# Optimization experiments

Measured on AMD Instinct MI355X. Metric: run time of the kernel, lower is better.

The kernel has to match this reference:

```python
import jax, jax.numpy as jnp
import numpy as np
from jax import lax

B = 16384
BN_EPS = 1e-5


def setup_inputs() -> dict:
    key = jax.random.key(0)
    ks = jax.random.split(key, 6)
    x = jax.random.normal(ks[0], (B, 1, 28, 28), jnp.float32)
    conv_w = jax.random.normal(ks[1], (4, 1, 3, 3), jnp.float32) * 0.2
    bn_gamma = jnp.ones((4,), jnp.float32)
    bn_beta = jnp.zeros((4,), jnp.float32)
    bn_mean = jnp.zeros((4,), jnp.float32)
    bn_var = jnp.ones((4,), jnp.float32)
    var_params = jax.random.normal(ks[2], (4,), jnp.float32)
    lin_w = jax.random.normal(ks[3], (10, 784), jnp.float32) * 0.03
    lin_b = jnp.zeros((10,), jnp.float32)
    return {"x": x, "conv_w": conv_w, "bn_gamma": bn_gamma, "bn_beta": bn_beta,
            "bn_mean": bn_mean, "bn_var": bn_var, "var_params": var_params,
            "lin_w": lin_w, "lin_b": lin_b}


def _ry_w0(s, theta):
    # apply RY(theta) to wire 0 (axis -2) of real state s[..., 2, 2]
    c, si = jnp.cos(theta * 0.5), jnp.sin(theta * 0.5)
    R = jnp.stack([jnp.stack([c, -si]), jnp.stack([si, c])])
    return jnp.einsum('ij,...jk->...ik', R, s)


def _ry_w1(s, theta):
    # apply RY(theta) to wire 1 (axis -1)
    c, si = jnp.cos(theta * 0.5), jnp.sin(theta * 0.5)
    R = jnp.stack([jnp.stack([c, -si]), jnp.stack([si, c])])
    return jnp.einsum('ij,...kj->...ki', R, s)


def _quantum_features(img, v):
    # img: [B, 28, 28] -> features [B, 196*4] (patch-major, 4 expvals each)
    b = img.shape[0]
    p = img.reshape(b, 14, 2, 14, 2).transpose(0, 1, 3, 2, 4)  # [B,14,14,2,2]
    # encoding RYs on same wire compose: angles a = p0+p2 (wire0), b = p1+p3 (wire1)
    ha = (p[..., 0, 0] + p[..., 1, 0]) * 0.5
    hb = (p[..., 0, 1] + p[..., 1, 1]) * 0.5
    w0 = jnp.stack([jnp.cos(ha), jnp.sin(ha)], axis=-1)
    w1 = jnp.stack([jnp.cos(hb), jnp.sin(hb)], axis=-1)
    s = w0[..., :, None] * w1[..., None, :]  # real statevector [B,14,14,2,2]
    # CNOT(control=0, target=1): flip wire1 where wire0 == 1
    s = jnp.stack([s[..., 0, :], s[..., 1, ::-1]], axis=-2)
    s = _ry_w0(s, v[0])
    s = _ry_w1(s, v[1])
    # CNOT(control=1, target=0): flip wire0 where wire1 == 1
    s = jnp.stack([s[..., :, 0], s[..., ::-1, 1]], axis=-1)
    s = _ry_w0(s, v[2])
    s = _ry_w1(s, v[3])
    z0 = jnp.sum(s[..., 0, :] ** 2 - s[..., 1, :] ** 2, axis=-1)
    z1 = jnp.sum(s[..., :, 0] ** 2 - s[..., :, 1] ** 2, axis=-1)
    x0 = 2.0 * jnp.sum(s[..., 0, :] * s[..., 1, :], axis=-1)
    x1 = 2.0 * jnp.sum(s[..., :, 0] * s[..., :, 1], axis=-1)
    return jnp.stack([z0, z1, x0, x1], axis=-1).reshape(b, -1)  # [B,784]


def reference(x, conv_w, bn_gamma, bn_beta, bn_mean, bn_var, var_params, lin_w, lin_b):
    b = x.shape[0]
    # classical branch: conv(s=2,p=1) -> BN (eval) -> ReLU -> flatten
    h = lax.conv_general_dilated(x, conv_w, window_strides=(2, 2),
                                 padding=((1, 1), (1, 1)))  # [B,4,14,14]
    inv = bn_gamma / jnp.sqrt(bn_var + BN_EPS)
    h = h * inv[None, :, None, None] + (bn_beta - bn_mean * inv)[None, :, None, None]
    h = jnp.maximum(h, 0.0)
    cls_out = h.reshape(b, -1)  # [B,784]
    # quantum branch over 2x2 patches
    q_out = _quantum_features(x[:, 0], var_params)  # [B,784]
    fused = cls_out + q_out
    logits = fused @ lin_w.T + lin_b
    return jax.nn.log_softmax(logits, axis=-1)
```

## Files before the change

kernel.cpp:

```cpp
#include <hip/hip_runtime.h>
#include <math.h>


#define NW 4
#define IMG_STRIDE 36
#define IMG_WORDS (29 * 36)

__device__ __forceinline__ void lds_fence() {
    asm volatile("s_waitcnt lgkmcnt(0)" ::: "memory");
}

__device__ __forceinline__ float wave64_sum(float x) {
    int v;
    v = __builtin_amdgcn_update_dpp(0, __float_as_int(x), 0x111, 0xf, 0xf, true); x += __int_as_float(v);
    v = __builtin_amdgcn_update_dpp(0, __float_as_int(x), 0x112, 0xf, 0xf, true); x += __int_as_float(v);
    v = __builtin_amdgcn_update_dpp(0, __float_as_int(x), 0x114, 0xf, 0xf, true); x += __int_as_float(v);
    v = __builtin_amdgcn_update_dpp(0, __float_as_int(x), 0x118, 0xf, 0xf, true); x += __int_as_float(v);
    v = __builtin_amdgcn_update_dpp(0, __float_as_int(x), 0x142, 0xa, 0xf, true); x += __int_as_float(v);
    v = __builtin_amdgcn_update_dpp(0, __float_as_int(x), 0x143, 0xc, 0xf, true); x += __int_as_float(v);
    return __int_as_float(__builtin_amdgcn_readlane(__float_as_int(x), 63));
}

__global__ __launch_bounds__(256, 4)
void quanv_fused(const float* __restrict__ x,
                 const float* __restrict__ conv_w,
                 const float* __restrict__ bn_gamma,
                 const float* __restrict__ bn_beta,
                 const float* __restrict__ bn_mean,
                 const float* __restrict__ bn_var,
                 const float* __restrict__ var_params,
                 const float* __restrict__ lin_w,
                 const float* __restrict__ lin_b,
                 float* __restrict__ out, int B)
{
    __shared__ __align__(16) float simg[NW][IMG_WORDS];
    __shared__ __align__(16) float scls[NW][784];

    const int tid  = threadIdx.x;
    const int wave = tid >> 6;
    const int lane = tid & 63;
    const int sample = blockIdx.x * NW + wave;
    const bool active = (sample < B);

    float* im = simg[wave];

    if (lane < 36) im[lane] = 0.f;
    if (lane < 28) im[(lane + 1) * IMG_STRIDE + 3] = 0.f;

    if (active) {
        const float4* xs = (const float4*)(x + (size_t)sample * 784);
        #pragma unroll
        for (int t = 0; t < 4; ++t) {
            int g = lane + t * 64;
            if (g < 196) {
                float4 v = xs[g];
                int row  = (unsigned)g / 7u;
                int colb = (g - row * 7) * 4;
                *(float4*)&im[(row + 1) * IMG_STRIDE + 4 + colb] = v;
            }
        }
    }

    float w[36];
    #pragma unroll
    for (int k = 0; k < 36; ++k) w[k] = conv_w[k];
    float inv[4], addc[4];
    #pragma unroll
    for (int c = 0; c < 4; ++c) {
        float iv = bn_gamma[c] * rsqrtf(bn_var[c] + 1e-5f);
        inv[c]  = iv;
        addc[c] = bn_beta[c] - bn_mean[c] * iv;
    }
    float cv[4], sv[4];
    #pragma unroll
    for (int k = 0; k < 4; ++k) __sincosf(var_params[k] * 0.5f, &sv[k], &cv[k]);

    lds_fence();

    float4 qf[4];
    #pragma unroll
    for (int t = 0; t < 4; ++t) qf[t] = make_float4(0.f, 0.f, 0.f, 0.f);

    if (active) {
        #pragma unroll
        for (int t = 0; t < 4; ++t) {
            int p = lane + t * 64;
            if (p < 196) {
                int i = (unsigned)p / 14u;
                int j = p - i * 14;
                int base = (2 * i) * IMG_STRIDE + 3 + 2 * j;
                float a00 = im[base + 0],                a01 = im[base + 1],                a02 = im[base + 2];
                float a10 = im[base + IMG_STRIDE + 0],   a11 = im[base + IMG_STRIDE + 1],   a12 = im[base + IMG_STRIDE + 2];
                float a20 = im[base + 2*IMG_STRIDE + 0], a21 = im[base + 2*IMG_STRIDE + 1], a22 = im[base + 2*IMG_STRIDE + 2];

                #pragma unroll
                for (int c = 0; c < 4; ++c) {
                    float h = w[c*9+0]*a00 + w[c*9+1]*a01 + w[c*9+2]*a02
                            + w[c*9+3]*a10 + w[c*9+4]*a11 + w[c*9+5]*a12
                            + w[c*9+6]*a20 + w[c*9+7]*a21 + w[c*9+8]*a22;
                    h = h * inv[c] + addc[c];
                    scls[wave][c * 196 + p] = fmaxf(h, 0.f);
                }

                float ha = 0.5f * (a11 + a21);
                float hb = 0.5f * (a12 + a22);
                float c0, s0, c1, s1;
                __sincosf(ha, &s0, &c0);
                __sincosf(hb, &s1, &c1);
                float m00 = c0*c1, m01 = c0*s1;
                float m10 = s0*s1, m11 = s0*c1;
                float t00 = cv[0]*m00 - sv[0]*m10, t01 = cv[0]*m01 - sv[0]*m11;
                float t10 = sv[0]*m00 + cv[0]*m10, t11 = sv[0]*m01 + cv[0]*m11;
                float u00 = cv[1]*t00 - sv[1]*t01, u01 = sv[1]*t00 + cv[1]*t01;
                float u10 = cv[1]*t10 - sv[1]*t11, u11 = sv[1]*t10 + cv[1]*t11;
                float tmp = u01; u01 = u11; u11 = tmp;
                float p00 = cv[2]*u00 - sv[2]*u10, p01 = cv[2]*u01 - sv[2]*u11;
                float p10 = sv[2]*u00 + cv[2]*u10, p11 = sv[2]*u01 + cv[2]*u11;
                float q00 = cv[3]*p00 - sv[3]*p01, q01 = sv[3]*p00 + cv[3]*p01;
                float q10 = cv[3]*p10 - sv[3]*p11, q11 = sv[3]*p10 + cv[3]*p11;

                float z0 = q00*q00 + q01*q01 - q10*q10 - q11*q11;
                float z1 = q00*q00 + q10*q10 - q01*q01 - q11*q11;
                float x0 = 2.f * (q00*q10 + q01*q11);
                float x1 = 2.f * (q00*q01 + q10*q11);
                qf[t] = make_float4(z0, z1, x0, x1);
            }
        }
    }

    lds_fence();

    if (active) {
        const float4* lw4 = (const float4*)lin_w;
        float ps[10];
        #pragma unroll
        for (int o = 0; o < 10; ++o) ps[o] = 0.f;

        #pragma unroll
        for (int t = 0; t < 4; ++t) {
            int p  = lane + t * 64;
            int pc = (p < 196) ? p : 195;
            float m = (p < 196) ? 1.f : 0.f;
            float4 cl = *(const float4*)&scls[wave][4 * pc];
            float4 f = make_float4((cl.x + qf[t].x) * m, (cl.y + qf[t].y) * m,
                                   (cl.z + qf[t].z) * m, (cl.w + qf[t].w) * m);
            #pragma unroll
            for (int o = 0; o < 10; ++o) {
                float4 wv = lw4[o * 196 + pc];
                ps[o] += f.x * wv.x + f.y * wv.y + f.z * wv.z + f.w * wv.w;
            }
        }

        float lg[10];
        #pragma unroll
        for (int o = 0; o < 10; ++o) lg[o] = wave64_sum(ps[o]) + lin_b[o];

        float mx = lg[0];
        #pragma unroll
        for (int o = 1; o < 10; ++o) mx = fmaxf(mx, lg[o]);
        float se = 0.f;
        #pragma unroll
        for (int o = 0; o < 10; ++o) se += __expf(lg[o] - mx);
        float ls = __logf(se);

        if (lane < 10) {
            float v = lg[0];
            #pragma unroll
            for (int o = 1; o < 10; ++o) v = (lane == o) ? lg[o] : v;
            out[(size_t)sample * 10 + lane] = v - mx - ls;
        }
    }
}

extern "C" void kernel_launch(void* const* d_in, const int* in_sizes, int n_in,
                              void* d_out, int out_size, void* d_ws, size_t ws_size,
                              hipStream_t stream) {
    const float* x          = (const float*)d_in[0];
    const float* conv_w     = (const float*)d_in[1];
    const float* bn_gamma   = (const float*)d_in[2];
    const float* bn_beta    = (const float*)d_in[3];
    const float* bn_mean    = (const float*)d_in[4];
    const float* bn_var     = (const float*)d_in[5];
    const float* var_params = (const float*)d_in[6];
    const float* lin_w      = (const float*)d_in[7];
    const float* lin_b      = (const float*)d_in[8];
    float* out = (float*)d_out;

    const int B = in_sizes[0] / 784;
    const int blocks = (B + NW - 1) / NW;
    quanv_fused<<<blocks, 256, 0, stream>>>(x, conv_w, bn_gamma, bn_beta, bn_mean,
                                            bn_var, var_params, lin_w, lin_b, out, B);
}
```

Measured before the change: 119.6 us.

## Process two samples per wave with fp16 LDS weights and dot2 reductions

Each wave now handles two samples, one per 32-lane half, and halves the block count. The linear weights are converted to fp16 in LDS once per block and combined with fdot2, replacing per-lane global float loads. The image is read directly from global memory with padding masks instead of being staged in LDS. Conv and quantum features are stored in fp16, and the final reduction uses a 32-lane DPP sum. The fp16 features and weights add precision loss, and each block pays for its own copy of the lin_w conversion.

```diff
diff --git a/kernel.cpp b/kernel.cpp
--- a/kernel.cpp
+++ b/kernel.cpp
@@ -3,22 +3,30 @@
 
 
 #define NW 4
-#define IMG_STRIDE 36
-#define IMG_WORDS (29 * 36)
-
-__device__ __forceinline__ void lds_fence() {
-    asm volatile("s_waitcnt lgkmcnt(0)" ::: "memory");
-}
-
-__device__ __forceinline__ float wave64_sum(float x) {
+#define SCLS_STRIDE 794
+
+typedef __fp16 h2 __attribute__((ext_vector_type(2)));
+typedef __fp16 h4 __attribute__((ext_vector_type(4)));
+
+#if __has_builtin(__builtin_amdgcn_fdot2)
+#define FDOT2(a, b, c) __builtin_amdgcn_fdot2((a), (b), (c), false)
+#else
+__device__ __forceinline__ float FDOT2(h2 a, h2 b, float c) {
+    return (float)a.x * (float)b.x + (float)a.y * (float)b.y + c;
+}
+#endif
+
+__device__ __forceinline__ float2 red32x2(float x) {
     int v;
     v = __builtin_amdgcn_update_dpp(0, __float_as_int(x), 0x111, 0xf, 0xf, true); x += __int_as_float(v);
     v = __builtin_amdgcn_update_dpp(0, __float_as_int(x), 0x112, 0xf, 0xf, true); x += __int_as_float(v);
     v = __builtin_amdgcn_update_dpp(0, __float_as_int(x), 0x114, 0xf, 0xf, true); x += __int_as_float(v);
     v = __builtin_amdgcn_update_dpp(0, __float_as_int(x), 0x118, 0xf, 0xf, true); x += __int_as_float(v);
     v = __builtin_amdgcn_update_dpp(0, __float_as_int(x), 0x142, 0xa, 0xf, true); x += __int_as_float(v);
-    v = __builtin_amdgcn_update_dpp(0, __float_as_int(x), 0x143, 0xc, 0xf, true); x += __int_as_float(v);
-    return __int_as_float(__builtin_amdgcn_readlane(__float_as_int(x), 63));
+    float2 r;
+    r.x = __int_as_float(__builtin_amdgcn_readlane(__float_as_int(x), 31));
+    r.y = __int_as_float(__builtin_amdgcn_readlane(__float_as_int(x), 63));
+    return r;
 }
 
 __global__ __launch_bounds__(256, 4)
@@ -33,30 +41,31 @@
                  const float* __restrict__ lin_b,
                  float* __restrict__ out, int B)
 {
-    __shared__ __align__(16) float simg[NW][IMG_WORDS];
-    __shared__ __align__(16) float scls[NW][784];
+    __shared__ __align__(16) __fp16 lwh[7840];
+    __shared__ __align__(16) __fp16 sclsAll[NW * 2 * SCLS_STRIDE];
 
     const int tid  = threadIdx.x;
     const int wave = tid >> 6;
     const int lane = tid & 63;
-    const int sample = blockIdx.x * NW + wave;
-    const bool active = (sample < B);
-
-    float* im = simg[wave];
-
-    if (lane < 36) im[lane] = 0.f;
-    if (lane < 28) im[(lane + 1) * IMG_STRIDE + 3] = 0.f;
-
-    if (active) {
-        const float4* xs = (const float4*)(x + (size_t)sample * 784);
+    const int half = lane >> 5;
+    const int l32  = lane & 31;
+
+    const int s  = blockIdx.x * (NW * 2) + wave * 2 + half;
+    const int sc = (s < B) ? s : (B - 1);
+    const float* xs = x + (size_t)sc * 784;
+    __fp16* myscls = &sclsAll[(wave * 2 + half) * SCLS_STRIDE];
+
+    {
+        const float4* src = (const float4*)lin_w;
         #pragma unroll
-        for (int t = 0; t < 4; ++t) {
-            int g = lane + t * 64;
-            if (g < 196) {
-                float4 v = xs[g];
-                int row  = (unsigned)g / 7u;
-                int colb = (g - row * 7) * 4;
-                *(float4*)&im[(row + 1) * IMG_STRIDE + 4 + colb] = v;
+        for (int t = 0; t < 8; ++t) {
+            int i = tid + t * 256;
+            if (i < 1960) {
+                float4 v = src[i];
+                h2 a = __builtin_amdgcn_cvt_pkrtz(v.x, v.y);
+                h2 b = __builtin_amdgcn_cvt_pkrtz(v.z, v.w);
+                h4 w4 = { a.x, a.y, b.x, b.y };
+                *(h4*)&lwh[4 * i] = w4;
             }
         }
     }
@@ -75,100 +84,118 @@
     #pragma unroll
     for (int k = 0; k < 4; ++k) __sincosf(var_params[k] * 0.5f, &sv[k], &cv[k]);
 
-    lds_fence();
-
-    float4 qf[4];
-    #pragma unroll
-    for (int t = 0; t < 4; ++t) qf[t] = make_float4(0.f, 0.f, 0.f, 0.f);
-
-    if (active) {
-        #pragma unroll
-        for (int t = 0; t < 4; ++t) {
-            int p = lane + t * 64;
-            if (p < 196) {
-                int i = (unsigned)p / 14u;
-                int j = p - i * 14;
-                int base = (2 * i) * IMG_STRIDE + 3 + 2 * j;
-                float a00 = im[base + 0],                a01 = im[base + 1],                a02 = im[base + 2];
-                float a10 = im[base + IMG_STRIDE + 0],   a11 = im[base + IMG_STRIDE + 1],   a12 = im[base + IMG_STRIDE + 2];
-                float a20 = im[base + 2*IMG_STRIDE + 0], a21 = im[base + 2*IMG_STRIDE + 1], a22 = im[base + 2*IMG_STRIDE + 2];
-
-                #pragma unroll
-                for (int c = 0; c < 4; ++c) {
-                    float h = w[c*9+0]*a00 + w[c*9+1]*a01 + w[c*9+2]*a02
-                            + w[c*9+3]*a10 + w[c*9+4]*a11 + w[c*9+5]*a12
-                            + w[c*9+6]*a20 + w[c*9+7]*a21 + w[c*9+8]*a22;
-                    h = h * inv[c] + addc[c];
-                    scls[wave][c * 196 + p] = fmaxf(h, 0.f);
-                }
-
-                float ha = 0.5f * (a11 + a21);
-                float hb = 0.5f * (a12 + a22);
-                float c0, s0, c1, s1;
-                __sincosf(ha, &s0, &c0);
-                __sincosf(hb, &s1, &c1);
-                float m00 = c0*c1, m01 = c0*s1;
-                float m10 = s0*s1, m11 = s0*c1;
-                float t00 = cv[0]*m00 - sv[0]*m10, t01 = cv[0]*m01 - sv[0]*m11;
-                float t10 = sv[0]*m00 + cv[0]*m10, t11 = sv[0]*m01 + cv[0]*m11;
-                float u00 = cv[1]*t00 - sv[1]*t01, u01 = sv[1]*t00 + cv[1]*t01;
-                float u10 = cv[1]*t10 - sv[1]*t11, u11 = sv[1]*t10 + cv[1]*t11;
-                float tmp = u01; u01 = u11; u11 = tmp;
-                float p00 = cv[2]*u00 - sv[2]*u10, p01 = cv[2]*u01 - sv[2]*u11;
-                float p10 = sv[2]*u00 + cv[2]*u10, p11 = sv[2]*u01 + cv[2]*u11;
-                float q00 = cv[3]*p00 - sv[3]*p01, q01 = sv[3]*p00 + cv[3]*p01;
-                float q10 = cv[3]*p10 - sv[3]*p11, q11 = sv[3]*p10 + cv[3]*p11;
-
-                float z0 = q00*q00 + q01*q01 - q10*q10 - q11*q11;
-                float z1 = q00*q00 + q10*q10 - q01*q01 - q11*q11;
-                float x0 = 2.f * (q00*q10 + q01*q11);
-                float x1 = 2.f * (q00*q01 + q10*q11);
-                qf[t] = make_float4(z0, z1, x0, x1);
+    h2 qh[7][2];
+    #pragma unroll
+    for (int t = 0; t < 7; ++t) {
+        int p = l32 + 32 * t;
+        bool act = (p < 196);
+        int pc = act ? p : 195;
+        unsigned i = (unsigned)pc / 14u;
+        int j = pc - (int)i * 14;
+        int omid = (int)(2 * i) * 28 + 2 * j;
+
+        float2 Rm = *(const float2*)(xs + omid);
+        float2 Rb = *(const float2*)(xs + omid + 28);
+        int ot = omid - 28; ot = (ot > 0) ? ot : 0;
+        float2 Rt = *(const float2*)(xs + ot);
+        int olt = omid - 30; olt = (olt > 0) ? olt : 0;
+        float2 Lt = *(const float2*)(xs + olt);
+        int olm = omid - 2; olm = (olm > 0) ? olm : 0;
+        float2 Lm = *(const float2*)(xs + olm);
+        float2 Lb = *(const float2*)(xs + olm + 28);
+
+        float mt = (i > 0) ? 1.f : 0.f;
+        float ml = (j > 0) ? 1.f : 0.f;
+        float a00 = Lt.y * (mt * ml), a01 = Rt.x * mt, a02 = Rt.y * mt;
+        float a10 = Lm.y * ml,        a11 = Rm.x,      a12 = Rm.y;
+        float a20 = Lb.y * ml,        a21 = Rb.x,      a22 = Rb.y;
+
+        if (act) {
+            #pragma unroll
+            for (int c = 0; c < 4; ++c) {
+                float h = w[c*9+0]*a00 + w[c*9+1]*a01 + w[c*9+2]*a02
+                        + w[c*9+3]*a10 + w[c*9+4]*a11 + w[c*9+5]*a12
+                        + w[c*9+6]*a20 + w[c*9+7]*a21 + w[c*9+8]*a22;
+                h = h * inv[c] + addc[c];
+                myscls[c * 196 + pc] = (__fp16)fmaxf(h, 0.f);
             }
         }
-    }
-
-    lds_fence();
-
-    if (active) {
-        const float4* lw4 = (const float4*)lin_w;
-        float ps[10];
+
+        float ha = 0.5f * (a11 + a21);
+        float hb = 0.5f * (a12 + a22);
+        float c0, s0, c1, s1;
+        __sincosf(ha, &s0, &c0);
+        __sincosf(hb, &s1, &c1);
+        float m00 = c0*c1, m01 = c0*s1;
+        float m10 = s0*s1, m11 = s0*c1;
+        float t00 = cv[0]*m00 - sv[0]*m10, t01 = cv[0]*m01 - sv[0]*m11;
+        float t10 = sv[0]*m00 + cv[0]*m10, t11 = sv[0]*m01 + cv[0]*m11;
+        float u00 = cv[1]*t00 - sv[1]*t01, u01 = sv[1]*t00 + cv[1]*t01;
+        float u10 = cv[1]*t10 - sv[1]*t11, u11 = sv[1]*t10 + cv[1]*t11;
+        float tmp = u01; u01 = u11; u11 = tmp;
+        float p00 = cv[2]*u00 - sv[2]*u10, p01 = cv[2]*u01 - sv[2]*u11;
+        float p10 = sv[2]*u00 + cv[2]*u10, p11 = sv[2]*u01 + cv[2]*u11;
+        float q00 = cv[3]*p00 - sv[3]*p01, q01 = sv[3]*p00 + cv[3]*p01;
+        float q10 = cv[3]*p10 - sv[3]*p11, q11 = sv[3]*p10 + cv[3]*p11;
+
+        float z0 = q00*q00 + q01*q01 - q10*q10 - q11*q11;
+        float z1 = q00*q00 + q10*q10 - q01*q01 - q11*q11;
+        float x0 = 2.f * (q00*q10 + q01*q11);
+        float x1 = 2.f * (q00*q01 + q10*q11);
+        qh[t][0] = __builtin_amdgcn_cvt_pkrtz(z0, z1);
+        qh[t][1] = __builtin_amdgcn_cvt_pkrtz(x0, x1);
+    }
+
+    __syncthreads();
+
+    float ps[10];
+    #pragma unroll
+    for (int o = 0; o < 10; ++o) ps[o] = 0.f;
+
+    const h2 hz = { (__fp16)0.f, (__fp16)0.f };
+    #pragma unroll
+    for (int t = 0; t < 7; ++t) {
+        int p = l32 + 32 * t;
+        bool act = (p < 196);
+        int pc = act ? p : 195;
+        h2 c0 = *(const h2*)&myscls[4 * pc];
+        h2 c1 = *(const h2*)&myscls[4 * pc + 2];
+        h2 f0 = c0 + qh[t][0];
+        h2 f1 = c1 + qh[t][1];
+        f0 = act ? f0 : hz;
+        f1 = act ? f1 : hz;
+        const __fp16* wbase = &lwh[4 * pc];
         #pragma unroll
-        for (int o = 0; o < 10; ++o) ps[o] = 0.f;
-
+        for (int o = 0; o < 10; ++o) {
+            h4 wv = *(const h4*)&wbase[o * 784];
+            h2 wlo = __builtin_shufflevector(wv, wv, 0, 1);
+            h2 whi = __builtin_shufflevector(wv, wv, 2, 3);
+            ps[o] = FDOT2(f0, wlo, ps[o]);
+            ps[o] = FDOT2(f1, whi, ps[o]);
+        }
+    }
+
+    float lg[10];
+    #pragma unroll
+    for (int o = 0; o < 10; ++o) {
+        float2 r = red32x2(ps[o]);
+        lg[o] = (half ? r.y : r.x) + lin_b[o];
+    }
+
+    float mx = lg[0];
+    #pragma unroll
+    for (int o = 1; o < 10; ++o) mx = fmaxf(mx, lg[o]);
+    float se = 0.f;
+    #pragma unroll
+    for (int o = 0; o < 10; ++o) se += __expf(lg[o] - mx);
+    float ls = __logf(se);
+
+    int o32 = l32;
+    if (o32 < 10 && s < B) {
+        float v = lg[0];
         #pragma unroll
-        for (int t = 0; t < 4; ++t) {
-            int p  = lane + t * 64;
-            int pc = (p < 196) ? p : 195;
-            float m = (p < 196) ? 1.f : 0.f;
-            float4 cl = *(const float4*)&scls[wave][4 * pc];
-            float4 f = make_float4((cl.x + qf[t].x) * m, (cl.y + qf[t].y) * m,
-                                   (cl.z + qf[t].z) * m, (cl.w + qf[t].w) * m);
-            #pragma unroll
-            for (int o = 0; o < 10; ++o) {
-                float4 wv = lw4[o * 196 + pc];
-                ps[o] += f.x * wv.x + f.y * wv.y + f.z * wv.z + f.w * wv.w;
-            }
-        }
-
-        float lg[10];
-        #pragma unroll
-        for (int o = 0; o < 10; ++o) lg[o] = wave64_sum(ps[o]) + lin_b[o];
-
-        float mx = lg[0];
-        #pragma unroll
-        for (int o = 1; o < 10; ++o) mx = fmaxf(mx, lg[o]);
-        float se = 0.f;
-        #pragma unroll
-        for (int o = 0; o < 10; ++o) se += __expf(lg[o] - mx);
-        float ls = __logf(se);
-
-        if (lane < 10) {
-            float v = lg[0];
-            #pragma unroll
-            for (int o = 1; o < 10; ++o) v = (lane == o) ? lg[o] : v;
-            out[(size_t)sample * 10 + lane] = v - mx - ls;
-        }
+        for (int o = 1; o < 10; ++o) v = (o32 == o) ? lg[o] : v;
+        out[(size_t)s * 10 + o32] = v - mx - ls;
     }
 }
 
@@ -187,7 +214,7 @@
     float* out = (float*)d_out;
 
     const int B = in_sizes[0] / 784;
-    const int blocks = (B + NW - 1) / NW;
+    const int blocks = (B + NW * 2 - 1) / (NW * 2);
     quanv_fused<<<blocks, 256, 0, stream>>>(x, conv_w, bn_gamma, bn_beta, bn_mean,
                                             bn_var, var_params, lin_w, lin_b, out, B);
 }
```

After: 110.7 us. 7.5% less time.
